# Performance work log

Hardware: AMD Instinct MI355X
Metric: run time of the kernel (lower is better)

Reference implementation:

```python
import jax, jax.numpy as jnp
import numpy as np

N = 100000
E = 1600000
IN_DIM = 128
HID = 128
OUT = 64
BN_EPS = 1e-5


def setup_inputs() -> dict:
    key = jax.random.key(0)
    ks = jax.random.split(key, 12)
    x = jax.random.normal(ks[0], (N, IN_DIM), dtype=jnp.float32)
    src = jax.random.randint(ks[1], (E,), 0, N, dtype=jnp.int64)
    dst = jax.random.randint(ks[2], (E,), 0, N, dtype=jnp.int64)
    edge_index = jnp.stack([src, dst], axis=0)
    def glorot(k, fan_in, fan_out):
        s = jnp.sqrt(6.0 / (fan_in + fan_out)).astype(jnp.float32)
        return jax.random.uniform(k, (fan_in, fan_out), jnp.float32, -s, s)
    return {
        "x": x,
        "edge_index": edge_index,
        "W1": glorot(ks[3], IN_DIM, HID), "b1": jnp.zeros((HID,), jnp.float32),
        "g1": jnp.ones((HID,), jnp.float32), "be1": jnp.zeros((HID,), jnp.float32),
        "W2": glorot(ks[4], HID, HID), "b2": jnp.zeros((HID,), jnp.float32),
        "g2": jnp.ones((HID,), jnp.float32), "be2": jnp.zeros((HID,), jnp.float32),
        "W3": glorot(ks[5], HID, OUT), "b3": jnp.zeros((OUT,), jnp.float32),
    }


def _gcn_norm(edge_index, n):
    # PyG GCNConv: add self-loops, symmetric normalization D^-1/2 (A+I) D^-1/2
    loop = jnp.arange(n, dtype=edge_index.dtype)
    src = jnp.concatenate([edge_index[0], loop])
    dst = jnp.concatenate([edge_index[1], loop])
    deg = jax.ops.segment_sum(jnp.ones_like(src, dtype=jnp.float32), dst, num_segments=n)
    dinv = jnp.where(deg > 0, jax.lax.rsqrt(deg), 0.0)
    norm = dinv[src] * dinv[dst]  # [E+N]
    return src, dst, norm


def _gcn(x, src, dst, norm, W, b, n):
    xw = x @ W                                  # [N, out]
    msg = xw[src] * norm[:, None]               # gather over edges
    return jax.ops.segment_sum(msg, dst, num_segments=n) + b


def _bn(x, g, be):
    # training-mode BatchNorm1d over node dim, biased variance
    mu = jnp.mean(x, axis=0)
    var = jnp.mean(jnp.square(x - mu), axis=0)
    return (x - mu) * jax.lax.rsqrt(var + BN_EPS) * g + be


def reference(x, edge_index, W1, b1, g1, be1, W2, b2, g2, be2, W3, b3):
    n = x.shape[0]
    src, dst, norm = _gcn_norm(edge_index, n)
    h = _gcn(x, src, dst, norm, W1, b1, n)
    h = jax.nn.relu(_bn(h, g1, be1))  # dropout = identity (eval)
    h = _gcn(h, src, dst, norm, W2, b2, n)
    h = jax.nn.relu(_bn(h, g2, be2))
    return _gcn(h, src, dst, norm, W3, b3, n)
```

## Files before the change

kernel.cpp:

```cpp
#include <hip/hip_runtime.h>
#include <cstdint>
#include <cstddef>

#define BN_EPS 1e-5f
#define BKT 256
#define BSH 9
#define CHUNK 8192

typedef __attribute__((ext_vector_type(8))) short bf16x8;
typedef __attribute__((ext_vector_type(4))) float f32x4;

__device__ __forceinline__ unsigned int f32_to_bf16_rne(float f) {
    unsigned int u = __float_as_uint(f);
    u += 0x7FFFu + ((u >> 16) & 1u);
    return u >> 16;
}
__device__ __forceinline__ unsigned int pack_bf16x2(float a, float b) {
    return f32_to_bf16_rne(a) | (f32_to_bf16_rne(b) << 16);
}
__device__ __forceinline__ float bf16_lo(unsigned int p) { return __uint_as_float(p << 16); }
__device__ __forceinline__ float bf16_hi(unsigned int p) { return __uint_as_float(p & 0xFFFF0000u); }

__global__ void hist_kernel(const int* __restrict__ dst, int* __restrict__ H, int e, int G) {
    __shared__ int h[BKT];
    int t = threadIdx.x, g = blockIdx.x;
    h[t] = 0;
    __syncthreads();
    int base = g * CHUNK;
#pragma unroll
    for (int i = 0; i < CHUNK / 256; i++) {
        int idx = base + i * 256 + t;
        if (idx < e) atomicAdd(&h[dst[idx] >> BSH], 1);
    }
    __syncthreads();
    H[t * G + g] = h[t];
}

__global__ void bin_scatter_kernel(const int* __restrict__ src, const int* __restrict__ dst,
                                   const int* __restrict__ Hscan, uint2* __restrict__ binned,
                                   int e, int G) {
    __shared__ int cur[BKT];
    int t = threadIdx.x, g = blockIdx.x;
    cur[t] = Hscan[t * G + g];
    __syncthreads();
    int base = g * CHUNK;
#pragma unroll
    for (int i = 0; i < CHUNK / 256; i++) {
        int idx = base + i * 256 + t;
        if (idx < e) {
            int s = src[idx], d = dst[idx];
            int pos = atomicAdd(&cur[d >> BSH], 1);
            uint2 v; v.x = (unsigned)s; v.y = (unsigned)d;
            binned[pos] = v;
        }
    }
}

__global__ __launch_bounds__(256) void bucket_build_kernel(const uint2* __restrict__ binned,
                                                           const int* __restrict__ Hscan,
                                                           int* __restrict__ cnt,
                                                           int* __restrict__ rowptr,
                                                           float* __restrict__ dinv,
                                                           int* __restrict__ esrc,
                                                           int e, int G, int n) {
    __shared__ int lcnt[512], lexc[512], ssum[256];
    const int t = threadIdx.x;
    const int b = blockIdx.x;
    const int start = Hscan[b * G];
    const int end = (b == BKT - 1) ? e : Hscan[(b + 1) * G];

    lcnt[t] = 0; lcnt[t + 256] = 0;
    __syncthreads();
    for (int i = start + t; i < end; i += 256)
        atomicAdd(&lcnt[binned[i].y & 511], 1);
    __syncthreads();

    int a0 = lcnt[2 * t], a1 = lcnt[2 * t + 1];
    ssum[t] = a0 + a1;
    __syncthreads();
    for (int off = 1; off < 256; off <<= 1) {
        int v = (t >= off) ? ssum[t - off] : 0;
        __syncthreads();
        ssum[t] += v;
        __syncthreads();
    }
    int excl = (t == 0) ? 0 : ssum[t - 1];
    lexc[2 * t] = excl;
    lexc[2 * t + 1] = excl + a0;
    __syncthreads();

    int nodebase = b << BSH;
#pragma unroll
    for (int j2 = 0; j2 < 2; j2++) {
        int j = 2 * t + j2;
        int node = nodebase + j;
        if (node < n) {
            int c = lcnt[j];
            cnt[node] = c;
            rowptr[node] = start + lexc[j];
            dinv[node] = rsqrtf((float)(c + 1));
        }
    }
    __syncthreads();

    for (int i = start + t; i < end; i += 256) {
        uint2 ed = binned[i];
        int pos = start + atomicAdd(&lexc[ed.y & 511], 1);
        esrc[pos] = (int)ed.x;
    }
}


__global__ void blocksum_kernel(const int* __restrict__ in, int* __restrict__ bsum, int n) {
    int t = threadIdx.x;
    int base = blockIdx.x * 1024 + t * 4;
    int s = 0;
    if (base + 3 < n) {
        int4 v = *(const int4*)&in[base];
        s = v.x + v.y + v.z + v.w;
    } else {
        for (int j = 0; j < 4; j++) if (base + j < n) s += in[base + j];
    }
    __shared__ int ls[256];
    ls[t] = s;
    __syncthreads();
    for (int off = 128; off > 0; off >>= 1) {
        if (t < off) ls[t] += ls[t + off];
        __syncthreads();
    }
    if (t == 0) bsum[blockIdx.x] = ls[0];
}

__global__ void scan_bsum_kernel(int* __restrict__ bsum, int nb) {
    int t = threadIdx.x;
    __shared__ int ls[256];
    int v = (t < nb) ? bsum[t] : 0;
    ls[t] = v;
    __syncthreads();
    for (int off = 1; off < 256; off <<= 1) {
        int p = (t >= off) ? ls[t - off] : 0;
        __syncthreads();
        ls[t] += p;
        __syncthreads();
    }
    if (t < nb) bsum[t] = ls[t] - v;
}

__global__ void scan_write1_kernel(const int* __restrict__ in, const int* __restrict__ bsum,
                                   int* __restrict__ out, int n) {
    int t = threadIdx.x;
    int base = blockIdx.x * 1024 + t * 4;
    int v[4];
    int s = 0;
    if (base + 3 < n) {
        int4 q = *(const int4*)&in[base];
        v[0] = q.x; v[1] = q.y; v[2] = q.z; v[3] = q.w;
        s = q.x + q.y + q.z + q.w;
    } else {
        for (int j = 0; j < 4; j++) { v[j] = (base + j < n) ? in[base + j] : 0; s += v[j]; }
    }
    __shared__ int ls[256];
    ls[t] = s;
    __syncthreads();
    for (int off = 1; off < 256; off <<= 1) {
        int p = (t >= off) ? ls[t - off] : 0;
        __syncthreads();
        ls[t] += p;
        __syncthreads();
    }
    int run = bsum[blockIdx.x] + ls[t] - s;
    if (base + 3 < n) {
        int4 r; r.x = run; r.y = run + v[0]; r.z = run + v[0] + v[1]; r.w = run + v[0] + v[1] + v[2];
        *(int4*)&out[base] = r;
    } else {
        for (int j = 0; j < 4; j++) {
            if (base + j < n) out[base + j] = run;
            run += v[j];
        }
    }
}


__device__ __forceinline__ void wprep_one(const float* __restrict__ W,
                                          uint4* __restrict__ whi, uint4* __restrict__ wlo,
                                          int slot, int OUTC) {
    int l  = slot & 63;
    int kc = (slot >> 6) & 3;
    int ct = slot >> 8;
    int c  = ct * 16 + (l & 15);
    int k0 = kc * 32 + (l >> 4) * 8;
    unsigned hi[4], lo[4];
#pragma unroll
    for (int jj = 0; jj < 4; jj++) {
        float v0 = W[(size_t)(k0 + 2 * jj) * OUTC + c];
        float v1 = W[(size_t)(k0 + 2 * jj + 1) * OUTC + c];
        unsigned h0 = f32_to_bf16_rne(v0), h1 = f32_to_bf16_rne(v1);
        float l0 = v0 - __uint_as_float(h0 << 16);
        float l1 = v1 - __uint_as_float(h1 << 16);
        hi[jj] = h0 | (h1 << 16);
        lo[jj] = pack_bf16x2(l0, l1);
    }
    uint4 uh; uh.x = hi[0]; uh.y = hi[1]; uh.z = hi[2]; uh.w = hi[3];
    uint4 ul; ul.x = lo[0]; ul.y = lo[1]; ul.z = lo[2]; ul.w = lo[3];
    whi[slot] = uh;
    wlo[slot] = ul;
}

__global__ void wprep_all_kernel(const float* __restrict__ W1, uint4* w1hi, uint4* w1lo,
                                 const float* __restrict__ W2, uint4* w2hi, uint4* w2lo,
                                 const float* __restrict__ W3, uint4* w3hi, uint4* w3lo) {
    int id = blockIdx.x * 256 + threadIdx.x;
    if (id < 2048)       wprep_one(W1, w1hi, w1lo, id, 128);
    else if (id < 4096)  wprep_one(W2, w2hi, w2lo, id - 2048, 128);
    else if (id < 5120)  wprep_one(W3, w3hi, w3lo, id - 4096, 64);
}


template <int OUTC, bool SLAB>
__global__ __launch_bounds__(256) void gemm_kernel(const float* __restrict__ X,
                                                   const uint4* __restrict__ whi,
                                                   const uint4* __restrict__ wlo,
                                                   const float* __restrict__ scale,
                                                   const float* __restrict__ shift,
                                                   const float* __restrict__ dinv,
                                                   unsigned int* __restrict__ Y, int n) {
    constexpr int NCT = OUTC / 16;
    constexpr int CTW = NCT / 4;
    __shared__ __align__(16) unsigned short lAhi[64 * 128];
    __shared__ __align__(16) unsigned short lAlo[64 * 128];
    __shared__ float ldv[64];
    const int t = threadIdx.x;
    const int base = blockIdx.x * 64;
    const int lane = t & 63;
    const int w = t >> 6;
    const bool bn = (scale != nullptr);

    if (t < 64) { int r = base + t; ldv[t] = (r < n) ? dinv[r] : 0.0f; }

    bf16x8 bhi[CTW][4], blo[CTW][4];
#pragma unroll
    for (int c = 0; c < CTW; c++) {
        int ct = w * CTW + c;
#pragma unroll
        for (int kc = 0; kc < 4; kc++) {
            int slot = (ct * 4 + kc) * 64 + lane;
            bhi[c][kc] = *reinterpret_cast<const bf16x8*>(whi + slot);
            blo[c][kc] = *reinterpret_cast<const bf16x8*>(wlo + slot);
        }
    }

    const int col4 = (t & 31) * 4;
    float4 sc4, sh4;
    if (bn) {
        sc4 = *(const float4*)&scale[col4];
        sh4 = *(const float4*)&shift[col4];
    }
#pragma unroll
    for (int i = 0; i < 8; i++) {
        int row = i * 8 + (t >> 5);
        int r = base + row;
        float4 xv = make_float4(0.f, 0.f, 0.f, 0.f);
        if (r < n) xv = *(const float4*)&X[(size_t)r * 128 + col4];
        if (bn) {
            xv.x = fmaxf(fmaf(xv.x, sc4.x, sh4.x), 0.0f);
            xv.y = fmaxf(fmaf(xv.y, sc4.y, sh4.y), 0.0f);
            xv.z = fmaxf(fmaf(xv.z, sc4.z, sh4.z), 0.0f);
            xv.w = fmaxf(fmaf(xv.w, sc4.w, sh4.w), 0.0f);
        }
        unsigned h0 = f32_to_bf16_rne(xv.x), h1 = f32_to_bf16_rne(xv.y);
        unsigned h2 = f32_to_bf16_rne(xv.z), h3 = f32_to_bf16_rne(xv.w);
        float l0 = xv.x - __uint_as_float(h0 << 16);
        float l1 = xv.y - __uint_as_float(h1 << 16);
        float l2 = xv.z - __uint_as_float(h2 << 16);
        float l3 = xv.w - __uint_as_float(h3 << 16);
        uint2 ph; ph.x = h0 | (h1 << 16); ph.y = h2 | (h3 << 16);
        uint2 pl; pl.x = pack_bf16x2(l0, l1); pl.y = pack_bf16x2(l2, l3);
        int off = row * 256 + ((col4 * 2) ^ ((row & 7) << 4));
        *(uint2*)((char*)lAhi + off) = ph;
        *(uint2*)((char*)lAlo + off) = pl;
    }
    __syncthreads();

    const int arow = lane & 15;
    const int kb16 = (lane >> 4) * 16;
#pragma unroll
    for (int rt = 0; rt < 4; rt++) {
        f32x4 acc[CTW];
#pragma unroll
        for (int c = 0; c < CTW; c++) acc[c] = (f32x4){0.f, 0.f, 0.f, 0.f};
        int row = rt * 16 + arow;
        int rb = row * 256;
        int sw = (row & 7) << 4;
#pragma unroll
        for (int kc = 0; kc < 4; kc++) {
            int off = rb + ((kc * 64 + kb16) ^ sw);
            bf16x8 ah = *(const bf16x8*)((const char*)lAhi + off);
            bf16x8 al = *(const bf16x8*)((const char*)lAlo + off);
#pragma unroll
            for (int c = 0; c < CTW; c++) {
                acc[c] = __builtin_amdgcn_mfma_f32_16x16x32_bf16(bhi[c][kc], ah, acc[c], 0, 0, 0);
                acc[c] = __builtin_amdgcn_mfma_f32_16x16x32_bf16(blo[c][kc], ah, acc[c], 0, 0, 0);
                acc[c] = __builtin_amdgcn_mfma_f32_16x16x32_bf16(bhi[c][kc], al, acc[c], 0, 0, 0);
            }
        }
        int r = base + row;
        if (r < n) {
            float dv = ldv[row];
#pragma unroll
            for (int c = 0; c < CTW; c++) {
                int ct = w * CTW + c;
                uint2 o;
                o.x = pack_bf16x2(acc[c][0] * dv, acc[c][1] * dv);
                o.y = pack_bf16x2(acc[c][2] * dv, acc[c][3] * dv);
                if constexpr (SLAB)
                    *(uint2*)&Y[(size_t)ct * n * 8 + (size_t)r * 8 + (lane >> 4) * 2] = o;
                else
                    *(uint2*)&Y[(size_t)r * (OUTC / 2) + ct * 8 + (lane >> 4) * 2] = o;
            }
        }
    }
}


__global__ __launch_bounds__(256) void agg128s_kernel(const unsigned int* __restrict__ xw,
                                                      const int* __restrict__ rowptr,
                                                      const int* __restrict__ cnt,
                                                      const int* __restrict__ esrc,
                                                      const float* __restrict__ dinv,
                                                      const float* __restrict__ bias,
                                                      float* __restrict__ out,
                                                      float* __restrict__ bnpart, int n) {
    __shared__ float lp[64][16], lq[64][16];
    __shared__ float lr[2][16][8];

    const uint2* xw2 = (const uint2*)xw;
    const int slab = blockIdx.x & 7;
    const int grp  = blockIdx.x >> 3;
    const int t = threadIdx.x;
    const int w = t >> 6;
    const int lane = t & 63;
    const int slot = lane >> 2;
    const int sub  = lane & 3;
    const int lnode = w * 16 + slot;
    const int node = grp * 64 + lnode;
    bool ok = node < n;
    int nc = ok ? node : 0;

    float di = dinv[nc];
    int beg = rowptr[nc];
    int cv  = ok ? cnt[nc] : 0;
    int last = beg + cv - 1;
    int nb = (cv + 7) >> 3;

    const size_t sbase = (size_t)slab * n * 4;
    uint2 ap = xw2[sbase + (size_t)nc * 4 + sub];
    float ax = bf16_lo(ap.x), ay = bf16_hi(ap.x);
    float az = bf16_lo(ap.y), aw = bf16_hi(ap.y);

    int s[8], sn[8];
    if (nb > 0) {
#pragma unroll
        for (int j = 0; j < 8; j++) {
            int idx = beg + j;
            s[j] = esrc[idx <= last ? idx : last];
        }
    }
    for (int b = 0; b < nb; b++) {
        int ebase = beg + b * 8;
        if (b + 1 < nb) {
#pragma unroll
            for (int j = 0; j < 8; j++) {
                int idx = ebase + 8 + j;
                sn[j] = esrc[idx <= last ? idx : last];
            }
        }
        uint2 v[8];
#pragma unroll
        for (int j = 0; j < 8; j++) v[j] = xw2[sbase + (size_t)s[j] * 4 + sub];
        int rem = last - ebase;
#pragma unroll
        for (int j = 0; j < 8; j++) {
            float m = (j <= rem) ? 1.0f : 0.0f;
            ax = fmaf(m, bf16_lo(v[j].x), ax);
            ay = fmaf(m, bf16_hi(v[j].x), ay);
            az = fmaf(m, bf16_lo(v[j].y), az);
            aw = fmaf(m, bf16_hi(v[j].y), aw);
        }
        if (b + 1 < nb) {
#pragma unroll
            for (int j = 0; j < 8; j++) s[j] = sn[j];
        }
    }

    float4 o = make_float4(0.f, 0.f, 0.f, 0.f);
    if (ok) {
        float4 bv = ((const float4*)bias)[slab * 4 + sub];
        o.x = fmaf(di, ax, bv.x);
        o.y = fmaf(di, ay, bv.y);
        o.z = fmaf(di, az, bv.z);
        o.w = fmaf(di, aw, bv.w);
        *(float4*)(out + (size_t)node * 128 + slab * 16 + sub * 4) = o;
    }

    int c0 = sub * 4;
    lp[lnode][c0 + 0] = o.x;  lq[lnode][c0 + 0] = o.x * o.x;
    lp[lnode][c0 + 1] = o.y;  lq[lnode][c0 + 1] = o.y * o.y;
    lp[lnode][c0 + 2] = o.z;  lq[lnode][c0 + 2] = o.z * o.z;
    lp[lnode][c0 + 3] = o.w;  lq[lnode][c0 + 3] = o.w * o.w;
    __syncthreads();
    {
        int col = t & 15;
        int which = (t >> 4) & 1;
        int chunk = t >> 5;
        float srd = 0.0f;
#pragma unroll
        for (int r = 0; r < 8; r++) {
            int rr = chunk * 8 + r;
            srd += which ? lq[rr][col] : lp[rr][col];
        }
        lr[which][col][chunk] = srd;
    }
    __syncthreads();
    if (t < 32) {
        int which = t >> 4;
        int col = t & 15;
        float srd = 0.0f;
#pragma unroll
        for (int c = 0; c < 8; c++) srd += lr[which][col][c];
        bnpart[(size_t)blockIdx.x * 32 + which * 16 + col] = srd;
    }
}


__global__ __launch_bounds__(256) void agg64_kernel(const unsigned int* __restrict__ xw,
                                                    const int* __restrict__ rowptr,
                                                    const int* __restrict__ cnt,
                                                    const int* __restrict__ esrc,
                                                    const float* __restrict__ dinv,
                                                    const float* __restrict__ bias,
                                                    float* __restrict__ out, int n) {
    int wid = (blockIdx.x * 256 + threadIdx.x) >> 6;
    int lane = threadIdx.x & 63;
    int half = lane >> 5;
    int hl = lane & 31;
    int node = wid * 2 + half;
    bool ok = node < n;
    int nc = ok ? node : 0;

    float di = dinv[nc];
    int beg = rowptr[nc];
    int cv  = ok ? cnt[nc] : 0;
    int last = beg + cv - 1;
    int nb = (cv + 7) >> 3;

    unsigned int ap = xw[(size_t)nc * 32 + hl];
    float ax = bf16_lo(ap), ay = bf16_hi(ap);

    int s[8], sn[8];
    if (nb > 0) {
#pragma unroll
        for (int j = 0; j < 8; j++) {
            int idx = beg + j;
            s[j] = esrc[idx <= last ? idx : last];
        }
    }
    for (int b = 0; b < nb; b++) {
        int ebase = beg + b * 8;
        if (b + 1 < nb) {
#pragma unroll
            for (int j = 0; j < 8; j++) {
                int idx = ebase + 8 + j;
                sn[j] = esrc[idx <= last ? idx : last];
            }
        }
        unsigned int v[8];
#pragma unroll
        for (int j = 0; j < 8; j++) v[j] = xw[(size_t)s[j] * 32 + hl];
        int rem = last - ebase;
#pragma unroll
        for (int j = 0; j < 8; j++) {
            float m = (j <= rem) ? 1.0f : 0.0f;
            ax = fmaf(m, bf16_lo(v[j]), ax);
            ay = fmaf(m, bf16_hi(v[j]), ay);
        }
        if (b + 1 < nb) {
#pragma unroll
            for (int j = 0; j < 8; j++) s[j] = sn[j];
        }
    }
    if (ok) {
        float2 bv = ((const float2*)bias)[hl];
        float2 o;
        o.x = fmaf(di, ax, bv.x);
        o.y = fmaf(di, ay, bv.y);
        ((float2*)(out + (size_t)node * 64))[hl] = o;
    }
}


__global__ void bnred_slab_kernel(const float* __restrict__ part, float* __restrict__ sums,
                                  int ngrp) {
    int t = threadIdx.x;
    int which = t >> 7;
    int c = t & 127;
    int slab = c >> 4, lcol = c & 15;
    float s = 0.0f;
    for (int k = blockIdx.x; k < ngrp; k += gridDim.x)
        s += part[(size_t)(k * 8 + slab) * 32 + which * 16 + lcol];
    atomicAdd(&sums[which * 128 + c], s);
}

__global__ void bn_finalize_kernel(const float* __restrict__ sums, const float* __restrict__ g,
                                   const float* __restrict__ be, float* __restrict__ scale,
                                   float* __restrict__ shift, int n) {
    int c = threadIdx.x;
    float inv_n = 1.0f / (float)n;
    float mean = sums[c] * inv_n;
    float var = sums[128 + c] * inv_n - mean * mean;
    float rstd = rsqrtf(var + BN_EPS);
    float sc = rstd * g[c];
    scale[c] = sc;
    shift[c] = be[c] - mean * sc;
}


extern "C" void kernel_launch(void* const* d_in, const int* in_sizes, int n_in,
                              void* d_out, int out_size, void* d_ws, size_t ws_size,
                              hipStream_t stream) {
    const float* x   = (const float*)d_in[0];
    const int*   ei  = (const int*)d_in[1];
    const float* W1  = (const float*)d_in[2];
    const float* b1  = (const float*)d_in[3];
    const float* g1  = (const float*)d_in[4];
    const float* be1 = (const float*)d_in[5];
    const float* W2  = (const float*)d_in[6];
    const float* b2  = (const float*)d_in[7];
    const float* g2  = (const float*)d_in[8];
    const float* be2 = (const float*)d_in[9];
    const float* W3  = (const float*)d_in[10];
    const float* b3  = (const float*)d_in[11];

    const int n = in_sizes[0] / 128;
    const int E = in_sizes[1] / 2;
    const int* srcv = ei;
    const int* dstv = ei + E;

    const int G = (E + CHUNK - 1) / CHUNK;
    const int HN = BKT * G;
    const int NB = (n + 511) >> 9;

    char* p = (char*)d_ws;
    auto carve = [&](size_t bytes) -> char* {
        char* q = p;
        p += (bytes + 255) & ~(size_t)255;
        return q;
    };
    int*   cnt    = (int*)carve((size_t)n * 4);
    int*   rowptr = (int*)carve((size_t)n * 4);
    float* dinv   = (float*)carve((size_t)n * 4);
    int*   esrc   = (int*)carve((size_t)E * 4);
    uint2* binned = (uint2*)carve((size_t)E * 8);
    int*   H      = (int*)carve((size_t)HN * 4);
    int*   Hscan  = (int*)carve((size_t)HN * 4);
    float* sums   = (float*)carve(512 * 4);
    float* bnsc   = (float*)carve(512 * 4);
    int*   bsum   = (int*)carve(1024 * 4);
    uint4* w1hi   = (uint4*)carve(2048 * 16);
    uint4* w1lo   = (uint4*)carve(2048 * 16);
    uint4* w2hi   = (uint4*)carve(2048 * 16);
    uint4* w2lo   = (uint4*)carve(2048 * 16);
    uint4* w3hi   = (uint4*)carve(1024 * 16);
    uint4* w3lo   = (uint4*)carve(1024 * 16);
    unsigned int* xwb = (unsigned int*)carve((size_t)n * 128 * 2);
    float* bufB   = (float*)carve((size_t)n * 128 * 4);

    float* bnpart = (float*)binned;

    hipMemsetAsync(sums, 0, 512 * 4, stream);

    int sbH = (HN + 1023) / 1024;

    wprep_all_kernel<<<20, 256, 0, stream>>>(W1, w1hi, w1lo, W2, w2hi, w2lo, W3, w3hi, w3lo);

    hist_kernel<<<G, 256, 0, stream>>>(dstv, H, E, G);
    blocksum_kernel<<<sbH, 256, 0, stream>>>(H, bsum, HN);
    scan_bsum_kernel<<<1, 256, 0, stream>>>(bsum, sbH);
    scan_write1_kernel<<<sbH, 256, 0, stream>>>(H, bsum, Hscan, HN);
    bin_scatter_kernel<<<G, 256, 0, stream>>>(srcv, dstv, Hscan, binned, E, G);
    bucket_build_kernel<<<NB, 256, 0, stream>>>(binned, Hscan, cnt, rowptr, dinv, esrc, E, G, n);

    int gb = (n + 63) / 64;
    int ngrp = (n + 63) / 64;
    int ab = (n + 7) / 8;

    gemm_kernel<128, true><<<gb, 256, 0, stream>>>(x, w1hi, w1lo, nullptr, nullptr, dinv, xwb, n);
    agg128s_kernel<<<ngrp * 8, 256, 0, stream>>>(xwb, rowptr, cnt, esrc, dinv, b1, bufB, bnpart, n);
    bnred_slab_kernel<<<64, 256, 0, stream>>>(bnpart, sums, ngrp);
    bn_finalize_kernel<<<1, 128, 0, stream>>>(sums, g1, be1, bnsc, bnsc + 128, n);

    gemm_kernel<128, true><<<gb, 256, 0, stream>>>(bufB, w2hi, w2lo, bnsc, bnsc + 128, dinv, xwb, n);
    agg128s_kernel<<<ngrp * 8, 256, 0, stream>>>(xwb, rowptr, cnt, esrc, dinv, b2, bufB, bnpart, n);
    bnred_slab_kernel<<<64, 256, 0, stream>>>(bnpart, sums + 256, ngrp);
    bn_finalize_kernel<<<1, 128, 0, stream>>>(sums + 256, g2, be2, bnsc + 256, bnsc + 384, n);

    gemm_kernel<64, false><<<gb, 256, 0, stream>>>(bufB, w3hi, w3lo, bnsc + 256, bnsc + 384, dinv, xwb, n);
    agg64_kernel<<<ab, 256, 0, stream>>>(xwb, rowptr, cnt, esrc, dinv, b3, (float*)d_out, n);
}
```

Baseline: 445.7 us.

## Sort nodes by in-degree so aggregation wavefronts process similar-degree nodes

Adds a counting sort of nodes by degree (histogram, scan, scatter) that builds a permutation plus permuted rowptr/cnt/dinv arrays. The aggregation kernels then iterate in permuted order, so lanes in a wavefront have similar edge counts, which cuts divergence and idle lanes in the 8-edge batch loop. It also pads the shared-memory BN tiles to 17 columns to avoid bank conflicts. The cost is three extra small kernels, and output writes and self-feature reads become scattered through perm instead of contiguous.

```diff
diff --git a/kernel.cpp b/kernel.cpp
--- a/kernel.cpp
+++ b/kernel.cpp
@@ -177,6 +177,63 @@
             if (base + j < n) out[base + j] = run;
             run += v[j];
         }
+    }
+}
+
+
+__global__ void dhist_kernel(const int* __restrict__ cnt, int* __restrict__ dh, int n) {
+    __shared__ int h[256];
+    int t = threadIdx.x;
+    h[t] = 0;
+    __syncthreads();
+    for (int i = blockIdx.x * 256 + t; i < n; i += gridDim.x * 256) {
+        int d = cnt[i];
+        atomicAdd(&h[d > 255 ? 255 : d], 1);
+    }
+    __syncthreads();
+    if (h[t]) atomicAdd(&dh[t], h[t]);
+}
+
+__global__ void dscan_kernel(const int* __restrict__ dh, int* __restrict__ cursor) {
+    int t = threadIdx.x;
+    __shared__ int ls[256];
+    int v = dh[t];
+    ls[t] = v;
+    __syncthreads();
+    for (int off = 1; off < 256; off <<= 1) {
+        int p = (t >= off) ? ls[t - off] : 0;
+        __syncthreads();
+        ls[t] += p;
+        __syncthreads();
+    }
+    cursor[t] = ls[t] - v;
+}
+
+__global__ void dscatter_kernel(const int* __restrict__ cnt, const int* __restrict__ rowptr,
+                                const float* __restrict__ dinv, int* __restrict__ cursor,
+                                int* __restrict__ perm, int* __restrict__ rowptr_p,
+                                int* __restrict__ cnt_p, float* __restrict__ dinv_p, int n) {
+    __shared__ int lh[256], lbase[256];
+    int t = threadIdx.x;
+    lh[t] = 0;
+    __syncthreads();
+    int i = blockIdx.x * 256 + t;
+    int d = 0, b = 0, lpos = 0;
+    bool ok = i < n;
+    if (ok) {
+        d = cnt[i];
+        b = d > 255 ? 255 : d;
+        lpos = atomicAdd(&lh[b], 1);
+    }
+    __syncthreads();
+    if (lh[t]) lbase[t] = atomicAdd(&cursor[t], lh[t]);
+    __syncthreads();
+    if (ok) {
+        int pos = lbase[b] + lpos;
+        perm[pos] = i;
+        rowptr_p[pos] = rowptr[i];
+        cnt_p[pos] = d;
+        dinv_p[pos] = dinv[i];
     }
 }
 
@@ -323,14 +380,15 @@
 
 
 __global__ __launch_bounds__(256) void agg128s_kernel(const unsigned int* __restrict__ xw,
-                                                      const int* __restrict__ rowptr,
-                                                      const int* __restrict__ cnt,
+                                                      const int* __restrict__ rowptr_p,
+                                                      const int* __restrict__ cnt_p,
                                                       const int* __restrict__ esrc,
-                                                      const float* __restrict__ dinv,
+                                                      const float* __restrict__ dinv_p,
+                                                      const int* __restrict__ perm,
                                                       const float* __restrict__ bias,
                                                       float* __restrict__ out,
                                                       float* __restrict__ bnpart, int n) {
-    __shared__ float lp[64][16], lq[64][16];
+    __shared__ float lp[64][17], lq[64][17];
     __shared__ float lr[2][16][8];
 
     const uint2* xw2 = (const uint2*)xw;
@@ -342,18 +400,19 @@
     const int slot = lane >> 2;
     const int sub  = lane & 3;
     const int lnode = w * 16 + slot;
-    const int node = grp * 64 + lnode;
-    bool ok = node < n;
-    int nc = ok ? node : 0;
-
-    float di = dinv[nc];
-    int beg = rowptr[nc];
-    int cv  = ok ? cnt[nc] : 0;
+    const int idx = grp * 64 + lnode;
+    bool ok = idx < n;
+    int ic = ok ? idx : 0;
+
+    float di = dinv_p[ic];
+    int beg = rowptr_p[ic];
+    int cv  = ok ? cnt_p[ic] : 0;
+    int node = perm[ic];
     int last = beg + cv - 1;
     int nb = (cv + 7) >> 3;
 
     const size_t sbase = (size_t)slab * n * 4;
-    uint2 ap = xw2[sbase + (size_t)nc * 4 + sub];
+    uint2 ap = xw2[sbase + (size_t)node * 4 + sub];
     float ax = bf16_lo(ap.x), ay = bf16_hi(ap.x);
     float az = bf16_lo(ap.y), aw = bf16_hi(ap.y);
 
@@ -361,8 +420,8 @@
     if (nb > 0) {
 #pragma unroll
         for (int j = 0; j < 8; j++) {
-            int idx = beg + j;
-            s[j] = esrc[idx <= last ? idx : last];
+            int i2 = beg + j;
+            s[j] = esrc[i2 <= last ? i2 : last];
         }
     }
     for (int b = 0; b < nb; b++) {
@@ -370,8 +429,8 @@
         if (b + 1 < nb) {
 #pragma unroll
             for (int j = 0; j < 8; j++) {
-                int idx = ebase + 8 + j;
-                sn[j] = esrc[idx <= last ? idx : last];
+                int i2 = ebase + 8 + j;
+                sn[j] = esrc[i2 <= last ? i2 : last];
             }
         }
         uint2 v[8];
@@ -433,35 +492,37 @@
 
 
 __global__ __launch_bounds__(256) void agg64_kernel(const unsigned int* __restrict__ xw,
-                                                    const int* __restrict__ rowptr,
-                                                    const int* __restrict__ cnt,
+                                                    const int* __restrict__ rowptr_p,
+                                                    const int* __restrict__ cnt_p,
                                                     const int* __restrict__ esrc,
-                                                    const float* __restrict__ dinv,
+                                                    const float* __restrict__ dinv_p,
+                                                    const int* __restrict__ perm,
                                                     const float* __restrict__ bias,
                                                     float* __restrict__ out, int n) {
     int wid = (blockIdx.x * 256 + threadIdx.x) >> 6;
     int lane = threadIdx.x & 63;
     int half = lane >> 5;
     int hl = lane & 31;
-    int node = wid * 2 + half;
-    bool ok = node < n;
-    int nc = ok ? node : 0;
-
-    float di = dinv[nc];
-    int beg = rowptr[nc];
-    int cv  = ok ? cnt[nc] : 0;
+    int idx = wid * 2 + half;
+    bool ok = idx < n;
+    int ic = ok ? idx : 0;
+
+    float di = dinv_p[ic];
+    int beg = rowptr_p[ic];
+    int cv  = ok ? cnt_p[ic] : 0;
+    int node = perm[ic];
     int last = beg + cv - 1;
     int nb = (cv + 7) >> 3;
 
-    unsigned int ap = xw[(size_t)nc * 32 + hl];
+    unsigned int ap = xw[(size_t)node * 32 + hl];
     float ax = bf16_lo(ap), ay = bf16_hi(ap);
 
     int s[8], sn[8];
     if (nb > 0) {
 #pragma unroll
         for (int j = 0; j < 8; j++) {
-            int idx = beg + j;
-            s[j] = esrc[idx <= last ? idx : last];
+            int i2 = beg + j;
+            s[j] = esrc[i2 <= last ? i2 : last];
         }
     }
     for (int b = 0; b < nb; b++) {
@@ -469,8 +530,8 @@
         if (b + 1 < nb) {
 #pragma unroll
             for (int j = 0; j < 8; j++) {
-                int idx = ebase + 8 + j;
-                sn[j] = esrc[idx <= last ? idx : last];
+                int i2 = ebase + 8 + j;
+                sn[j] = esrc[i2 <= last ? i2 : last];
             }
         }
         unsigned int v[8];
@@ -565,6 +626,11 @@
     float* sums   = (float*)carve(512 * 4);
     float* bnsc   = (float*)carve(512 * 4);
     int*   bsum   = (int*)carve(1024 * 4);
+    int*   dh     = (int*)carve(512 * 4);
+    int*   perm   = (int*)carve((size_t)n * 4);
+    int*   rowptr_p = (int*)carve((size_t)n * 4);
+    int*   cnt_p  = (int*)carve((size_t)n * 4);
+    float* dinv_p = (float*)carve((size_t)n * 4);
     uint4* w1hi   = (uint4*)carve(2048 * 16);
     uint4* w1lo   = (uint4*)carve(2048 * 16);
     uint4* w2hi   = (uint4*)carve(2048 * 16);
@@ -575,8 +641,10 @@
     float* bufB   = (float*)carve((size_t)n * 128 * 4);
 
     float* bnpart = (float*)binned;
+    int* cursor = dh + 256;
 
     hipMemsetAsync(sums, 0, 512 * 4, stream);
+    hipMemsetAsync(dh, 0, 512 * 4, stream);
 
     int sbH = (HN + 1023) / 1024;
 
@@ -589,20 +657,26 @@
     bin_scatter_kernel<<<G, 256, 0, stream>>>(srcv, dstv, Hscan, binned, E, G);
     bucket_build_kernel<<<NB, 256, 0, stream>>>(binned, Hscan, cnt, rowptr, dinv, esrc, E, G, n);
 
+    int nblk = (n + 255) / 256;
+    dhist_kernel<<<128, 256, 0, stream>>>(cnt, dh, n);
+    dscan_kernel<<<1, 256, 0, stream>>>(dh, cursor);
+    dscatter_kernel<<<nblk, 256, 0, stream>>>(cnt, rowptr, dinv, cursor,
+                                              perm, rowptr_p, cnt_p, dinv_p, n);
+
     int gb = (n + 63) / 64;
     int ngrp = (n + 63) / 64;
     int ab = (n + 7) / 8;
 
     gemm_kernel<128, true><<<gb, 256, 0, stream>>>(x, w1hi, w1lo, nullptr, nullptr, dinv, xwb, n);
-    agg128s_kernel<<<ngrp * 8, 256, 0, stream>>>(xwb, rowptr, cnt, esrc, dinv, b1, bufB, bnpart, n);
+    agg128s_kernel<<<ngrp * 8, 256, 0, stream>>>(xwb, rowptr_p, cnt_p, esrc, dinv_p, perm, b1, bufB, bnpart, n);
     bnred_slab_kernel<<<64, 256, 0, stream>>>(bnpart, sums, ngrp);
     bn_finalize_kernel<<<1, 128, 0, stream>>>(sums, g1, be1, bnsc, bnsc + 128, n);
 
     gemm_kernel<128, true><<<gb, 256, 0, stream>>>(bufB, w2hi, w2lo, bnsc, bnsc + 128, dinv, xwb, n);
-    agg128s_kernel<<<ngrp * 8, 256, 0, stream>>>(xwb, rowptr, cnt, esrc, dinv, b2, bufB, bnpart, n);
+    agg128s_kernel<<<ngrp * 8, 256, 0, stream>>>(xwb, rowptr_p, cnt_p, esrc, dinv_p, perm, b2, bufB, bnpart, n);
     bnred_slab_kernel<<<64, 256, 0, stream>>>(bnpart, sums + 256, ngrp);
     bn_finalize_kernel<<<1, 128, 0, stream>>>(sums + 256, g2, be2, bnsc + 256, bnsc + 384, n);
 
     gemm_kernel<64, false><<<gb, 256, 0, stream>>>(bufB, w3hi, w3lo, bnsc + 256, bnsc + 384, dinv, xwb, n);
-    agg64_kernel<<<ab, 256, 0, stream>>>(xwb, rowptr, cnt, esrc, dinv, b3, (float*)d_out, n);
-}
+    agg64_kernel<<<ab, 256, 0, stream>>>(xwb, rowptr_p, cnt_p, esrc, dinv_p, perm, b3, (float*)d_out, n);
+}
```

After: 491.1 us. 10.2% more time.
